# Kernel optimization log

Measured on AMD Instinct MI355X. Metric: run time of the kernel, lower is better.

## Reference

```python
import jax, jax.numpy as jnp
import numpy as np

N_HEAD = 16
EPS = 1e-6


def _rope(x, cos, sin):
    # x: [B, T, H, D]; cos/sin: [1, T, 1, D//2]
    d = x.shape[-1] // 2
    x1, x2 = x[..., :d], x[..., d:]
    return jnp.concatenate([x1 * cos + x2 * sin, -x1 * sin + x2 * cos], axis=-1)


def _rmsnorm(x):
    # parameter-free RMSNorm over last dim
    return x * jax.lax.rsqrt(jnp.mean(x * x, axis=-1, keepdims=True) + EPS)


def setup_inputs() -> dict:
    key = jax.random.key(0)
    ks = jax.random.split(key, 5)
    B, T, C = 4, 2048, 1024
    d_half = (C // N_HEAD) // 2
    x = jax.random.normal(ks[0], (B, T, C), dtype=jnp.float32)
    # realistic rotary tables
    inv_freq = 1.0 / (10000.0 ** (np.arange(d_half, dtype=np.float32) / d_half))
    t = np.arange(T, dtype=np.float32)
    freqs = np.outer(t, inv_freq)  # [T, d_half]
    cos = jnp.asarray(np.cos(freqs))[None, :, None, :]
    sin = jnp.asarray(np.sin(freqs))[None, :, None, :]
    w_attn = jax.random.normal(ks[1], (3 * C, C), dtype=jnp.float32) * 0.02
    w_proj = jax.random.normal(ks[2], (C, C), dtype=jnp.float32) * 0.02
    return {"x": x, "cos": cos, "sin": sin, "w_attn": w_attn, "w_proj": w_proj}


def reference(x, cos, sin, w_attn, w_proj):
    B, T, C = x.shape
    H = N_HEAD
    D = C // H
    qkv = x @ w_attn.T  # [B, T, 3C]
    q, k, v = jnp.split(qkv, 3, axis=2)
    q = q.reshape(B, T, H, D)
    k = k.reshape(B, T, H, D)
    v = v.reshape(B, T, H, D)
    q = _rmsnorm(_rope(q, cos, sin))
    k = _rmsnorm(_rope(k, cos, sin))
    # causal SDPA
    scale = 1.0 / jnp.sqrt(jnp.asarray(D, dtype=x.dtype))
    scores = jnp.einsum("bqhd,bkhd->bhqk", q, k) * scale  # [B, H, T, T]
    causal = jnp.tril(jnp.ones((T, T), dtype=bool))
    scores = jnp.where(causal[None, None], scores, jnp.asarray(-jnp.inf, dtype=scores.dtype))
    att = jax.nn.softmax(scores, axis=-1)
    y = jnp.einsum("bhqk,bkhd->bqhd", att, v).reshape(B, T, C)
    return y @ w_proj.T
```

## Files before the change

### kernel.cpp

```cpp
#include <hip/hip_runtime.h>
#include <hip/hip_bf16.h>
#include <math.h>


#define TT 2048
#define CC 1024
#define HH 16
#define DD 64

typedef __attribute__((ext_vector_type(8))) short short8;
typedef __attribute__((ext_vector_type(4))) short short4_t;
typedef __attribute__((ext_vector_type(4))) float f32x4;
typedef unsigned short ushort_t;

__device__ __forceinline__ ushort_t f2bf(float f) {
    unsigned u = __builtin_bit_cast(unsigned, f);
    u = (u + 0x7fffu + ((u >> 16) & 1u)) >> 16;
    return (ushort_t)u;
}

__global__ __launch_bounds__(256) void cast_bf16(const float* __restrict__ in,
                                                 ushort_t* __restrict__ out, int n8) {
    const int i = blockIdx.x * 256 + threadIdx.x;
    if (i >= n8) return;
    const float4* p = (const float4*)in + (size_t)i * 2;
    float4 f0 = p[0], f1 = p[1];
    short8 v;
    v[0] = (short)f2bf(f0.x); v[1] = (short)f2bf(f0.y);
    v[2] = (short)f2bf(f0.z); v[3] = (short)f2bf(f0.w);
    v[4] = (short)f2bf(f1.x); v[5] = (short)f2bf(f1.y);
    v[6] = (short)f2bf(f1.z); v[7] = (short)f2bf(f1.w);
    *(short8*)(out + (size_t)i * 8) = v;
}

template <bool OUTF32>
__global__ __launch_bounds__(256) void gemm_bt(const ushort_t* __restrict__ A,
                                               const ushort_t* __restrict__ B,
                                               void* __restrict__ C,
                                               int M, int N, int K, int lda) {
    __shared__ ushort_t As[128 * 32];
    __shared__ ushort_t Bs[128 * 32];

    const int tid  = threadIdx.x;
    const int wv   = tid >> 6;
    const int ln   = tid & 63;
    const int quad = ln >> 4;
    const int lm   = ln & 15;
    const int wm   = wv & 1;
    const int wn   = wv >> 1;
    const int rowC = blockIdx.y * 128;
    const int colC = blockIdx.x * 128;

    const int srow = wv * 16 + (ln >> 2);
    const int skq  = (ln & 3) * 8;

    f32x4 acc[4][4];
#pragma unroll
    for (int i = 0; i < 4; ++i)
#pragma unroll
        for (int j = 0; j < 4; ++j) acc[i][j] = (f32x4){0.f, 0.f, 0.f, 0.f};

    for (int k0 = 0; k0 < K; k0 += 32) {
        __syncthreads();
#pragma unroll
        for (int half = 0; half < 2; ++half) {
            const ushort_t* gA = A + (size_t)(rowC + half * 64 + srow) * lda + k0 + skq;
            const ushort_t* gB = B + (size_t)(colC + half * 64 + srow) * K + k0 + skq;
            ushort_t* lA = As + (half * 64 + wv * 16) * 32;
            ushort_t* lB = Bs + (half * 64 + wv * 16) * 32;
            __builtin_amdgcn_global_load_lds(
                (const __attribute__((address_space(1))) unsigned int*)gA,
                (__attribute__((address_space(3))) unsigned int*)lA, 16, 0, 0);
            __builtin_amdgcn_global_load_lds(
                (const __attribute__((address_space(1))) unsigned int*)gB,
                (__attribute__((address_space(3))) unsigned int*)lB, 16, 0, 0);
        }
        __syncthreads();

        short8 af[4], bf[4];
#pragma unroll
        for (int mt = 0; mt < 4; ++mt)
            af[mt] = *(const short8*)&As[(wm * 64 + mt * 16 + lm) * 32 + quad * 8];
#pragma unroll
        for (int nt = 0; nt < 4; ++nt)
            bf[nt] = *(const short8*)&Bs[(wn * 64 + nt * 16 + lm) * 32 + quad * 8];
#pragma unroll
        for (int mt = 0; mt < 4; ++mt)
#pragma unroll
            for (int nt = 0; nt < 4; ++nt)
                acc[mt][nt] = __builtin_amdgcn_mfma_f32_16x16x32_bf16(
                    af[mt], bf[nt], acc[mt][nt], 0, 0, 0);
    }

#pragma unroll
    for (int mt = 0; mt < 4; ++mt)
#pragma unroll
        for (int r = 0; r < 4; ++r) {
            const size_t row = rowC + wm * 64 + mt * 16 + quad * 4 + r;
#pragma unroll
            for (int nt = 0; nt < 4; ++nt) {
                const size_t col = colC + wn * 64 + nt * 16 + lm;
                if (OUTF32) ((float*)C)[row * N + col] = acc[mt][nt][r];
                else        ((ushort_t*)C)[row * N + col] = f2bf(acc[mt][nt][r]);
            }
        }
}

__global__ __launch_bounds__(256) void gemm_qkv(const ushort_t* __restrict__ A,
                                                const ushort_t* __restrict__ B,
                                                ushort_t* __restrict__ C,
                                                ushort_t* __restrict__ vtb,
                                                const float* __restrict__ cosb,
                                                const float* __restrict__ sinb,
                                                int M, int N, int K) {
    __shared__ ushort_t As[128 * 32];
    __shared__ ushort_t Bs[128 * 32];

    const int tid  = threadIdx.x;
    const int wv   = tid >> 6;
    const int ln   = tid & 63;
    const int quad = ln >> 4;
    const int lm   = ln & 15;
    const int wm   = wv & 1;
    const int wn   = wv >> 1;
    const int rowC = blockIdx.y * 128;
    const int colC = blockIdx.x * 128;

    const int srow = wv * 16 + (ln >> 2);
    const int skq  = (ln & 3) * 8;

    f32x4 acc[4][4];
#pragma unroll
    for (int i = 0; i < 4; ++i)
#pragma unroll
        for (int j = 0; j < 4; ++j) acc[i][j] = (f32x4){0.f, 0.f, 0.f, 0.f};

    for (int k0 = 0; k0 < K; k0 += 32) {
        __syncthreads();
#pragma unroll
        for (int half = 0; half < 2; ++half) {
            const ushort_t* gA = A + (size_t)(rowC + half * 64 + srow) * K + k0 + skq;
            const ushort_t* gB = B + (size_t)(colC + half * 64 + srow) * K + k0 + skq;
            ushort_t* lA = As + (half * 64 + wv * 16) * 32;
            ushort_t* lB = Bs + (half * 64 + wv * 16) * 32;
            __builtin_amdgcn_global_load_lds(
                (const __attribute__((address_space(1))) unsigned int*)gA,
                (__attribute__((address_space(3))) unsigned int*)lA, 16, 0, 0);
            __builtin_amdgcn_global_load_lds(
                (const __attribute__((address_space(1))) unsigned int*)gB,
                (__attribute__((address_space(3))) unsigned int*)lB, 16, 0, 0);
        }
        __syncthreads();

        short8 af[4], bf[4];
#pragma unroll
        for (int mt = 0; mt < 4; ++mt)
            af[mt] = *(const short8*)&As[(wm * 64 + mt * 16 + lm) * 32 + quad * 8];
#pragma unroll
        for (int nt = 0; nt < 4; ++nt)
            bf[nt] = *(const short8*)&Bs[(wn * 64 + nt * 16 + lm) * 32 + quad * 8];
#pragma unroll
        for (int mt = 0; mt < 4; ++mt)
#pragma unroll
            for (int nt = 0; nt < 4; ++nt)
                acc[mt][nt] = __builtin_amdgcn_mfma_f32_16x16x32_bf16(
                    af[mt], bf[nt], acc[mt][nt], 0, 0, 0);
    }

    const bool isqk = colC < 2 * CC;
    if (isqk) {
#pragma unroll
        for (int mt = 0; mt < 4; ++mt)
#pragma unroll
            for (int r = 0; r < 4; ++r) {
                const int row = rowC + wm * 64 + mt * 16 + quad * 4 + r;
                ushort_t* Cp = C + (size_t)row * N + colC + wn * 64 + lm;
                const int t = row & (TT - 1);
                float ss = 0.f;
#pragma unroll
                for (int nt = 0; nt < 4; ++nt) ss += acc[mt][nt][r] * acc[mt][nt][r];
                ss += __shfl_xor(ss, 1);
                ss += __shfl_xor(ss, 2);
                ss += __shfl_xor(ss, 4);
                ss += __shfl_xor(ss, 8);
                const float rinv = rsqrtf(ss * (1.0f / 64.0f) + 1e-6f);
                const float c0 = cosb[t * 32 + lm];
                const float c1 = cosb[t * 32 + 16 + lm];
                const float s0 = sinb[t * 32 + lm];
                const float s1 = sinb[t * 32 + 16 + lm];
                const float o0 = acc[mt][0][r] * c0 + acc[mt][2][r] * s0;
                const float o1 = acc[mt][1][r] * c1 + acc[mt][3][r] * s1;
                const float o2 = acc[mt][2][r] * c0 - acc[mt][0][r] * s0;
                const float o3 = acc[mt][3][r] * c1 - acc[mt][1][r] * s1;
                Cp[0]  = f2bf(o0 * rinv);
                Cp[16] = f2bf(o1 * rinv);
                Cp[32] = f2bf(o2 * rinv);
                Cp[48] = f2bf(o3 * rinv);
            }
    } else {
#pragma unroll
        for (int mt = 0; mt < 4; ++mt) {
            const int row0 = rowC + wm * 64 + mt * 16 + quad * 4;
            const int bb = row0 >> 11;
            const int tt = row0 & (TT - 1);
#pragma unroll
            for (int nt = 0; nt < 4; ++nt) {
                const int hd = colC - 2 * CC + wn * 64 + nt * 16 + lm;
                short4_t pk;
                pk[0] = (short)f2bf(acc[mt][nt][0]);
                pk[1] = (short)f2bf(acc[mt][nt][1]);
                pk[2] = (short)f2bf(acc[mt][nt][2]);
                pk[3] = (short)f2bf(acc[mt][nt][3]);
                *(short4_t*)(vtb + (size_t)(bb * CC + hd) * TT + tt) = pk;
            }
        }
    }
}

__global__ __launch_bounds__(256, 3) void attn_mfma(ushort_t* __restrict__ qkv,
                                                    const ushort_t* __restrict__ vt) {
    const int qp = blockIdx.x;
    const int h  = blockIdx.y;
    const int b  = blockIdx.z;
    const int tid  = threadIdx.x;
    const int w    = tid >> 6;
    const int lane = tid & 63;
    const int quad = lane >> 4;
    const int lm   = lane & 15;
    const int qtA = qp, qtB = 31 - qp;

    __shared__ ushort_t Ks[64][72];
    __shared__ ushort_t Vt[64][72];
    __shared__ ushort_t Ps[4][16][72];

    short8 qfA[2], qfB[2];
    {
        const ushort_t* qa = qkv + (size_t)(b * TT + qtA * 64 + w * 16 + lm) * (3 * CC) + h * DD;
        const ushort_t* qb = qkv + (size_t)(b * TT + qtB * 64 + w * 16 + lm) * (3 * CC) + h * DD;
        qfA[0] = *(const short8*)(qa + quad * 8);
        qfA[1] = *(const short8*)(qa + 32 + quad * 8);
        qfB[0] = *(const short8*)(qb + quad * 8);
        qfB[1] = *(const short8*)(qb + 32 + quad * 8);
    }

    f32x4 OA[4], OB[4];
#pragma unroll
    for (int dt = 0; dt < 4; ++dt) {
        OA[dt] = (f32x4){0.f, 0.f, 0.f, 0.f};
        OB[dt] = (f32x4){0.f, 0.f, 0.f, 0.f};
    }
    float psA[4] = {0.f, 0.f, 0.f, 0.f};
    float psB[4] = {0.f, 0.f, 0.f, 0.f};

    const int sn = tid >> 2;
    const int sd = (tid & 3) * 16;

    auto process = [&](const short8 (&qf)[2], const short8 (&kf)[2][4],
                       const short8 (&vf)[2][4], f32x4 (&O)[4], float (&ps)[4],
                       bool diag) {
        f32x4 sf[4];
#pragma unroll
        for (int nt = 0; nt < 4; ++nt) sf[nt] = (f32x4){0.f, 0.f, 0.f, 0.f};
#pragma unroll
        for (int kk = 0; kk < 2; ++kk)
#pragma unroll
            for (int nt = 0; nt < 4; ++nt)
                sf[nt] = __builtin_amdgcn_mfma_f32_16x16x32_bf16(qf[kk], kf[kk][nt],
                                                                 sf[nt], 0, 0, 0);
#pragma unroll
        for (int r = 0; r < 4; ++r) {
            const int rloc = w * 16 + quad * 4 + r;
            const int m = quad * 4 + r;
#pragma unroll
            for (int nt = 0; nt < 4; ++nt) {
                const int n = nt * 16 + lm;
                float s = sf[nt][r] * 0.125f - 8.f;
                if (diag) s = (n <= rloc) ? s : -1e30f;
                const float p = __expf(s);
                ps[r] += p;
                Ps[w][m][(((n >> 3) ^ (m >> 2)) << 3) | (n & 7)] = f2bf(p);
            }
        }
#pragma unroll
        for (int kk = 0; kk < 2; ++kk) {
            const short8 pf =
                *(const short8*)&Ps[w][lm][(((kk * 4 + quad) ^ (lm >> 2)) << 3)];
#pragma unroll
            for (int dt = 0; dt < 4; ++dt)
                O[dt] = __builtin_amdgcn_mfma_f32_16x16x32_bf16(pf, vf[kk][dt],
                                                                O[dt], 0, 0, 0);
        }
    };

    for (int kt = 0; kt <= qtB; ++kt) {
        __syncthreads();
        {
            const ushort_t* kp = qkv + (size_t)(b * TT + kt * 64 + sn) * (3 * CC) + CC + h * DD + sd;
            *(short8*)&Ks[sn][sd]     = *(const short8*)kp;
            *(short8*)&Ks[sn][sd + 8] = *(const short8*)(kp + 8);
            const ushort_t* vp = vt + (size_t)(b * CC + h * DD + sn) * TT + kt * 64 + sd;
            *(short8*)&Vt[sn][sd]     = *(const short8*)vp;
            *(short8*)&Vt[sn][sd + 8] = *(const short8*)(vp + 8);
        }
        __syncthreads();

        short8 kf[2][4], vf[2][4];
#pragma unroll
        for (int kk = 0; kk < 2; ++kk)
#pragma unroll
            for (int i = 0; i < 4; ++i) {
                kf[kk][i] = *(const short8*)&Ks[i * 16 + lm][kk * 32 + quad * 8];
                vf[kk][i] = *(const short8*)&Vt[i * 16 + lm][kk * 32 + quad * 8];
            }

        if (kt <= qtA) process(qfA, kf, vf, OA, psA, kt == qtA);
        process(qfB, kf, vf, OB, psB, kt == qtB);
    }

    auto epi = [&](f32x4 (&O)[4], float (&ps)[4], int qt) {
#pragma unroll
        for (int r = 0; r < 4; ++r) {
            float l = ps[r];
            l += __shfl_xor(l, 1);
            l += __shfl_xor(l, 2);
            l += __shfl_xor(l, 4);
            l += __shfl_xor(l, 8);
            const float inv_l = 1.f / l;
            ushort_t* yp = qkv + (size_t)(b * TT + qt * 64 + w * 16 + quad * 4 + r) * (3 * CC)
                               + 2 * CC + h * DD + lm;
#pragma unroll
            for (int dt = 0; dt < 4; ++dt) yp[dt * 16] = f2bf(O[dt][r] * inv_l);
        }
    };
    epi(OA, psA, qtA);
    epi(OB, psB, qtB);
}

extern "C" void kernel_launch(void* const* d_in, const int* in_sizes, int n_in,
                              void* d_out, int out_size, void* d_ws, size_t ws_size,
                              hipStream_t stream) {
    const float* x      = (const float*)d_in[0];
    const float* cosb   = (const float*)d_in[1];
    const float* sinb   = (const float*)d_in[2];
    const float* w_attn = (const float*)d_in[3];
    const float* w_proj = (const float*)d_in[4];
    float* out = (float*)d_out;

    ushort_t* qkvb = (ushort_t*)d_ws;
    ushort_t* vtb  = qkvb + (size_t)8192 * 3072;
    ushort_t* xb   = vtb  + (size_t)8192 * 1024;
    ushort_t* wab  = xb   + (size_t)8192 * 1024;
    ushort_t* wpb  = wab  + (size_t)3072 * 1024;

    cast_bf16<<<(8192 * 1024 / 8 + 255) / 256, 256, 0, stream>>>(x, xb, 8192 * 1024 / 8);
    cast_bf16<<<(3072 * 1024 / 8 + 255) / 256, 256, 0, stream>>>(w_attn, wab, 3072 * 1024 / 8);
    cast_bf16<<<(1024 * 1024 / 8 + 255) / 256, 256, 0, stream>>>(w_proj, wpb, 1024 * 1024 / 8);

    gemm_qkv<<<dim3(3072 / 128, 8192 / 128), 256, 0, stream>>>(
        xb, wab, qkvb, vtb, cosb, sinb, 8192, 3072, 1024);

    attn_mfma<<<dim3(16, HH, 4), 256, 0, stream>>>(qkvb, vtb);

    gemm_bt<true><<<dim3(1024 / 128, 8192 / 128), 256, 0, stream>>>(
        qkvb + 2 * CC, wpb, out, 8192, 1024, 1024, 3 * CC);
}
```

Baseline: 309.5 us.

## Restructure causal attention: one query tile per block, double-buffered K/V, register P

```diff
diff --git a/kernel.cpp b/kernel.cpp
--- a/kernel.cpp
+++ b/kernel.cpp
@@ -11,6 +11,7 @@
 typedef __attribute__((ext_vector_type(8))) short short8;
 typedef __attribute__((ext_vector_type(4))) short short4_t;
 typedef __attribute__((ext_vector_type(4))) float f32x4;
+typedef __attribute__((ext_vector_type(4))) int int4v;
 typedef unsigned short ushort_t;
 
 __device__ __forceinline__ ushort_t f2bf(float f) {
@@ -219,7 +220,7 @@
 
 __global__ __launch_bounds__(256, 3) void attn_mfma(ushort_t* __restrict__ qkv,
                                                     const ushort_t* __restrict__ vt) {
-    const int qp = blockIdx.x;
+    const int qt = 31 - (int)blockIdx.x;
     const int h  = blockIdx.y;
     const int b  = blockIdx.z;
     const int tid  = threadIdx.x;
@@ -227,113 +228,125 @@
     const int lane = tid & 63;
     const int quad = lane >> 4;
     const int lm   = lane & 15;
-    const int qtA = qp, qtB = 31 - qp;
-
-    __shared__ ushort_t Ks[64][72];
-    __shared__ ushort_t Vt[64][72];
-    __shared__ ushort_t Ps[4][16][72];
-
-    short8 qfA[2], qfB[2];
+    const int qloc = w * 16 + lm;
+
+    __shared__ ushort_t Ks[2][64][72];
+    __shared__ ushort_t Vs[2][64][72];
+
+    short8 qf[2];
     {
-        const ushort_t* qa = qkv + (size_t)(b * TT + qtA * 64 + w * 16 + lm) * (3 * CC) + h * DD;
-        const ushort_t* qb = qkv + (size_t)(b * TT + qtB * 64 + w * 16 + lm) * (3 * CC) + h * DD;
-        qfA[0] = *(const short8*)(qa + quad * 8);
-        qfA[1] = *(const short8*)(qa + 32 + quad * 8);
-        qfB[0] = *(const short8*)(qb + quad * 8);
-        qfB[1] = *(const short8*)(qb + 32 + quad * 8);
-    }
-
-    f32x4 OA[4], OB[4];
-#pragma unroll
-    for (int dt = 0; dt < 4; ++dt) {
-        OA[dt] = (f32x4){0.f, 0.f, 0.f, 0.f};
-        OB[dt] = (f32x4){0.f, 0.f, 0.f, 0.f};
-    }
-    float psA[4] = {0.f, 0.f, 0.f, 0.f};
-    float psB[4] = {0.f, 0.f, 0.f, 0.f};
+        const ushort_t* qa = qkv + (size_t)(b * TT + qt * 64 + w * 16 + lm) * (3 * CC) + h * DD;
+        qf[0] = *(const short8*)(qa + quad * 8);
+        qf[1] = *(const short8*)(qa + 32 + quad * 8);
+    }
+
+    f32x4 O[4];
+#pragma unroll
+    for (int dt = 0; dt < 4; ++dt) O[dt] = (f32x4){0.f, 0.f, 0.f, 0.f};
+    f32x4 lac = (f32x4){0.f, 0.f, 0.f, 0.f};
+
+    const short one_bf = (short)0x3F80;
+    const short8 vones = {one_bf, one_bf, one_bf, one_bf, one_bf, one_bf, one_bf, one_bf};
 
     const int sn = tid >> 2;
-    const int sd = (tid & 3) * 16;
-
-    auto process = [&](const short8 (&qf)[2], const short8 (&kf)[2][4],
-                       const short8 (&vf)[2][4], f32x4 (&O)[4], float (&ps)[4],
-                       bool diag) {
+    const int si = tid & 3;
+    const int sd = si * 16;
+    const int kb = ((si >> 1) << 5) + ((si & 1) << 2);
+
+    short8 k0v, k1v, v0v, v1v;
+    auto stage_load = [&](int kt) {
+        const ushort_t* kp = qkv + (size_t)(b * TT + kt * 64 + sn) * (3 * CC) + CC + h * DD + sd;
+        k0v = *(const short8*)kp;
+        k1v = *(const short8*)(kp + 8);
+        const ushort_t* vp = vt + (size_t)(b * CC + h * DD + sn) * TT + kt * 64 + sd;
+        v0v = *(const short8*)vp;
+        v1v = *(const short8*)(vp + 8);
+    };
+    auto stage_write = [&](int bf) {
+        *(short8*)&Ks[bf][sn][sd]     = k0v;
+        *(short8*)&Ks[bf][sn][sd + 8] = k1v;
+        *(short4_t*)&Vs[bf][sn][kb]      = __builtin_shufflevector(v0v, v0v, 0, 1, 2, 3);
+        *(short4_t*)&Vs[bf][sn][kb + 8]  = __builtin_shufflevector(v0v, v0v, 4, 5, 6, 7);
+        *(short4_t*)&Vs[bf][sn][kb + 16] = __builtin_shufflevector(v1v, v1v, 0, 1, 2, 3);
+        *(short4_t*)&Vs[bf][sn][kb + 24] = __builtin_shufflevector(v1v, v1v, 4, 5, 6, 7);
+    };
+
+    auto softmax_pack = [&](const f32x4 (&sf)[4], short8 (&pa)[2], bool diag) {
+        int dw[8];
+#pragma unroll
+        for (int i = 0; i < 4; ++i) {
+            float pv[4];
+#pragma unroll
+            for (int r = 0; r < 4; ++r) {
+                const float s = fmaf(sf[i][r], 0.125f, -8.0f);
+                float p = __expf(s);
+                if (diag) {
+                    const int kloc = i * 16 + quad * 4 + r;
+                    p = (kloc <= qloc) ? p : 0.0f;
+                }
+                pv[r] = p;
+            }
+            asm("v_cvt_pk_bf16_f32 %0, %1, %2" : "=v"(dw[i * 2 + 0]) : "v"(pv[0]), "v"(pv[1]));
+            asm("v_cvt_pk_bf16_f32 %0, %1, %2" : "=v"(dw[i * 2 + 1]) : "v"(pv[2]), "v"(pv[3]));
+        }
+        int4v w0 = {dw[0], dw[1], dw[2], dw[3]};
+        int4v w1 = {dw[4], dw[5], dw[6], dw[7]};
+        pa[0] = __builtin_bit_cast(short8, w0);
+        pa[1] = __builtin_bit_cast(short8, w1);
+    };
+
+    stage_load(0);
+    stage_write(0);
+    __syncthreads();
+
+    int cur = 0;
+    for (int kt = 0; kt <= qt; ++kt) {
+        if (kt < qt) stage_load(kt + 1);
+
+        short8 kf[2][4];
+#pragma unroll
+        for (int kk = 0; kk < 2; ++kk)
+#pragma unroll
+            for (int i = 0; i < 4; ++i)
+                kf[kk][i] = *(const short8*)&Ks[cur][i * 16 + lm][kk * 32 + quad * 8];
+
         f32x4 sf[4];
 #pragma unroll
-        for (int nt = 0; nt < 4; ++nt) sf[nt] = (f32x4){0.f, 0.f, 0.f, 0.f};
+        for (int i = 0; i < 4; ++i) sf[i] = (f32x4){0.f, 0.f, 0.f, 0.f};
 #pragma unroll
         for (int kk = 0; kk < 2; ++kk)
 #pragma unroll
-            for (int nt = 0; nt < 4; ++nt)
-                sf[nt] = __builtin_amdgcn_mfma_f32_16x16x32_bf16(qf[kk], kf[kk][nt],
-                                                                 sf[nt], 0, 0, 0);
-#pragma unroll
-        for (int r = 0; r < 4; ++r) {
-            const int rloc = w * 16 + quad * 4 + r;
-            const int m = quad * 4 + r;
-#pragma unroll
-            for (int nt = 0; nt < 4; ++nt) {
-                const int n = nt * 16 + lm;
-                float s = sf[nt][r] * 0.125f - 8.f;
-                if (diag) s = (n <= rloc) ? s : -1e30f;
-                const float p = __expf(s);
-                ps[r] += p;
-                Ps[w][m][(((n >> 3) ^ (m >> 2)) << 3) | (n & 7)] = f2bf(p);
-            }
-        }
+            for (int i = 0; i < 4; ++i)
+                sf[i] = __builtin_amdgcn_mfma_f32_16x16x32_bf16(kf[kk][i], qf[kk],
+                                                                sf[i], 0, 0, 0);
+
+        short8 pa[2];
+        if (kt == qt) softmax_pack(sf, pa, true);
+        else          softmax_pack(sf, pa, false);
+
 #pragma unroll
         for (int kk = 0; kk < 2; ++kk) {
-            const short8 pf =
-                *(const short8*)&Ps[w][lm][(((kk * 4 + quad) ^ (lm >> 2)) << 3)];
-#pragma unroll
-            for (int dt = 0; dt < 4; ++dt)
-                O[dt] = __builtin_amdgcn_mfma_f32_16x16x32_bf16(pf, vf[kk][dt],
-                                                                O[dt], 0, 0, 0);
-        }
-    };
-
-    for (int kt = 0; kt <= qtB; ++kt) {
-        __syncthreads();
-        {
-            const ushort_t* kp = qkv + (size_t)(b * TT + kt * 64 + sn) * (3 * CC) + CC + h * DD + sd;
-            *(short8*)&Ks[sn][sd]     = *(const short8*)kp;
-            *(short8*)&Ks[sn][sd + 8] = *(const short8*)(kp + 8);
-            const ushort_t* vp = vt + (size_t)(b * CC + h * DD + sn) * TT + kt * 64 + sd;
-            *(short8*)&Vt[sn][sd]     = *(const short8*)vp;
-            *(short8*)&Vt[sn][sd + 8] = *(const short8*)(vp + 8);
-        }
-        __syncthreads();
-
-        short8 kf[2][4], vf[2][4];
-#pragma unroll
-        for (int kk = 0; kk < 2; ++kk)
-#pragma unroll
-            for (int i = 0; i < 4; ++i) {
-                kf[kk][i] = *(const short8*)&Ks[i * 16 + lm][kk * 32 + quad * 8];
-                vf[kk][i] = *(const short8*)&Vt[i * 16 + lm][kk * 32 + quad * 8];
-            }
-
-        if (kt <= qtA) process(qfA, kf, vf, OA, psA, kt == qtA);
-        process(qfB, kf, vf, OB, psB, kt == qtB);
-    }
-
-    auto epi = [&](f32x4 (&O)[4], float (&ps)[4], int qt) {
-#pragma unroll
-        for (int r = 0; r < 4; ++r) {
-            float l = ps[r];
-            l += __shfl_xor(l, 1);
-            l += __shfl_xor(l, 2);
-            l += __shfl_xor(l, 4);
-            l += __shfl_xor(l, 8);
-            const float inv_l = 1.f / l;
-            ushort_t* yp = qkv + (size_t)(b * TT + qt * 64 + w * 16 + quad * 4 + r) * (3 * CC)
-                               + 2 * CC + h * DD + lm;
-#pragma unroll
-            for (int dt = 0; dt < 4; ++dt) yp[dt * 16] = f2bf(O[dt][r] * inv_l);
-        }
-    };
-    epi(OA, psA, qtA);
-    epi(OB, psB, qtB);
+#pragma unroll
+            for (int dt = 0; dt < 4; ++dt) {
+                const short8 vf = *(const short8*)&Vs[cur][dt * 16 + lm][kk * 32 + quad * 8];
+                O[dt] = __builtin_amdgcn_mfma_f32_16x16x32_bf16(pa[kk], vf, O[dt], 0, 0, 0);
+            }
+            lac = __builtin_amdgcn_mfma_f32_16x16x32_bf16(pa[kk], vones, lac, 0, 0, 0);
+        }
+
+        if (kt < qt) stage_write(cur ^ 1);
+        __syncthreads();
+        cur ^= 1;
+    }
+
+#pragma unroll
+    for (int r = 0; r < 4; ++r) {
+        const float inv_l = 1.0f / lac[r];
+        ushort_t* yp = qkv + (size_t)(b * TT + qt * 64 + w * 16 + quad * 4 + r) * (3 * CC)
+                           + 2 * CC + h * DD + lm;
+#pragma unroll
+        for (int dt = 0; dt < 4; ++dt) yp[dt * 16] = f2bf(O[dt][r] * inv_l);
+    }
 }
 
 extern "C" void kernel_launch(void* const* d_in, const int* in_sizes, int n_in,
@@ -359,7 +372,7 @@
     gemm_qkv<<<dim3(3072 / 128, 8192 / 128), 256, 0, stream>>>(
         xb, wab, qkvb, vtb, cosb, sinb, 8192, 3072, 1024);
 
-    attn_mfma<<<dim3(16, HH, 4), 256, 0, stream>>>(qkvb, vtb);
+    attn_mfma<<<dim3(32, HH, 4), 256, 0, stream>>>(qkvb, vtb);
 
     gemm_bt<true><<<dim3(1024 / 128, 8192 / 128), 256, 0, stream>>>(
         qkvb + 2 * CC, wpb, out, 8192, 1024, 1024, 3 * CC);
```

After: 312.3 us. About the same (+0.9%).
